# Performance work log

Measured on AMD Instinct MI355X. Metric: run time of the kernel, lower is better.

The kernel has to match this reference:

```python
import jax, jax.numpy as jnp
import numpy as np

MARGIN = 1.0
EPS = 1e-11


def setup_inputs() -> dict:
    key = jax.random.key(0)
    k1, k2, k3 = jax.random.split(key, 3)
    B, D, C = 8192, 512, 128
    features = jax.random.normal(k1, (B, D), dtype=jnp.float32)
    labels = jax.random.randint(k2, (B,), 0, C, dtype=jnp.int64)
    neg_u = jax.random.uniform(k3, (B,), dtype=jnp.float32)
    return {"features": features, "labels": labels, "neg_u": neg_u}


def reference(features, labels, neg_u):
    n = features.shape[0]
    sq = jnp.sum(features * features, axis=1)  # [n]
    d2 = sq[:, None] + sq[None, :] - 2.0 * (features @ features.T)
    dist = jnp.sqrt(jnp.clip(d2, EPS, None))  # [n, n]

    same = labels[:, None] == labels[None, :]
    eye = jnp.eye(n, dtype=bool)
    pos_mask = same & ~eye           # valid positives per anchor
    neg_mask = ~same                 # valid negatives per anchor
    n_neg = neg_mask.sum(axis=1)     # [n]

    # deterministic "random" negative: pick the floor(u * n_neg)-th negative
    # (stable argsort puts negatives first, preserving original order)
    order = jnp.argsort(jnp.where(neg_mask, 0, 1), axis=1, stable=True)  # [n, n]
    k = jnp.floor(neg_u * n_neg.astype(neg_u.dtype)).astype(jnp.int32)
    k = jnp.clip(k, 0, jnp.maximum(n_neg - 1, 0).astype(jnp.int32))
    neg_idx = jnp.take_along_axis(order, k[:, None], axis=1)[:, 0]       # [n]
    neg_dist = dist[jnp.arange(n), neg_idx]                               # [n]

    # MarginRankingLoss(y=1): max(0, margin + pos_dist - neg_dist), per (anchor, pos) pair
    valid = pos_mask & (n_neg > 0)[:, None]
    per_pair = jnp.maximum(MARGIN + dist - neg_dist[:, None], 0.0)
    counter = valid.sum()
    total = jnp.where(valid, per_pair, 0.0).sum()
    return total / counter.astype(total.dtype)
```

## Files before the change

### kernel.cpp

```cpp
#include <hip/hip_runtime.h>
#include <hip/hip_bf16.h>
#include <cstdint>

#define NN 8192
#define DD 512
#define NC 128

typedef unsigned short u16;
typedef __attribute__((ext_vector_type(8))) short short8;
typedef __attribute__((ext_vector_type(4))) float f32x4;

#define AS1 __attribute__((address_space(1)))
#define AS3 __attribute__((address_space(3)))

#define FB_OFF   ((size_t)0)
#define SQ_OFF   (FB_OFF + (size_t)NN*DD*2)
#define ND_OFF   (SQ_OFF + (size_t)NN*4)
#define ACC_OFF  (ND_OFF + (size_t)NN*4)
#define CC_OFF   (ACC_OFF + 64)
#define POS_OFF  (CC_OFF + 1024)

__global__ __launch_bounds__(256) void k_prep(const float* __restrict__ F,
    u16* __restrict__ Fb, float* __restrict__ sq, int* __restrict__ accz) {
  if (blockIdx.x == 0 && threadIdx.x < 16) accz[threadIdx.x] = 0;
  const int wid = threadIdx.x >> 6, lane = threadIdx.x & 63;
  const int row = blockIdx.x * 4 + wid;
  const float* fr = F + (size_t)row * DD + lane * 8;
  float4 v0 = *(const float4*)fr;
  float4 v1 = *(const float4*)(fr + 4);
  float s = v0.x*v0.x + v0.y*v0.y + v0.z*v0.z + v0.w*v0.w
          + v1.x*v1.x + v1.y*v1.y + v1.z*v1.z + v1.w*v1.w;
  #pragma unroll
  for (int o = 32; o; o >>= 1) s += __shfl_xor(s, o);
  float t[8] = {v0.x, v0.y, v0.z, v0.w, v1.x, v1.y, v1.z, v1.w};
  unsigned p[8];
  #pragma unroll
  for (int e = 0; e < 8; ++e) {
    unsigned b = __float_as_uint(t[e]);
    b += 0x7fffu + ((b >> 16) & 1u);
    p[e] = b >> 16;
  }
  uint4 w;
  w.x = p[0] | (p[1] << 16); w.y = p[2] | (p[3] << 16);
  w.z = p[4] | (p[5] << 16); w.w = p[6] | (p[7] << 16);
  *(uint4*)(Fb + (size_t)row * DD + lane * 8) = w;
  if (lane == 0) sq[row] = s;
}

__global__ __launch_bounds__(256) void k_classpos(const int* __restrict__ labels,
    int* __restrict__ cc, int* __restrict__ pos, int* __restrict__ cnt) {
  const int c = blockIdx.x;
  const int wid = threadIdx.x >> 6, lane = threadIdx.x & 63;
  __shared__ int wcnt[4], woff[4];
  const int base0 = wid * 2048;
  int cw = 0;
  for (int b = 0; b < 2048; b += 64)
    cw += __popcll(__ballot(labels[base0 + b + lane] == c));
  if (lane == 0) wcnt[wid] = cw;
  __syncthreads();
  if (threadIdx.x == 0) {
    int o = 0;
    #pragma unroll
    for (int w = 0; w < 4; ++w) { woff[w] = o; o += wcnt[w]; }
    cc[c] = o;
    if (o < NN) atomicAdd(cnt, o * (o - 1));
  }
  __syncthreads();
  int off = woff[wid];
  for (int b = 0; b < 2048; b += 64) {
    const int idx = base0 + b + lane;
    const int hit = (labels[idx] == c);
    const unsigned long long m = __ballot(hit);
    if (hit) pos[c * 128 + off + __popcll(m & ((1ull << lane) - 1ull))] = idx;
    off += __popcll(m);
  }
  __syncthreads();
  const int nc = cc[c];
  for (int t = nc + threadIdx.x; t < 128; t += 256) pos[c * 128 + t] = 0;
}

__global__ __launch_bounds__(256) void k_neg2(const float* __restrict__ F,
    const float* __restrict__ sq, const int* __restrict__ labels,
    const float* __restrict__ negu, const int* __restrict__ cc,
    const int* __restrict__ pos, float* __restrict__ nd) {
  const int wid = threadIdx.x >> 6, lane = threadIdx.x & 63;
  const int i = blockIdx.x * 4 + wid;
  const int c = labels[i];
  const int nc = cc[c];
  const int n_neg = NN - nc;
  if (n_neg <= 0) { if (lane == 0) nd[i] = __builtin_inff(); return; }
  int k = (int)floorf(negu[i] * (float)n_neg);
  k = k < 0 ? 0 : (k > n_neg - 1 ? n_neg - 1 : k);
  const int* pc = pos + c * 128;
  const int p0 = pc[lane], p1 = pc[64 + lane];
  const int t = __popcll(__ballot((lane < nc) && (p0 - lane <= k)))
              + __popcll(__ballot((64 + lane < nc) && (p1 - (64 + lane) <= k)));
  const int j = k + t;
  const float* fi = F + (size_t)i * DD + lane * 8;
  const float* fj = F + (size_t)j * DD + lane * 8;
  float4 a0 = *(const float4*)fi, a1 = *(const float4*)(fi + 4);
  float4 b0 = *(const float4*)fj, b1 = *(const float4*)(fj + 4);
  float d = a0.x*b0.x + a0.y*b0.y + a0.z*b0.z + a0.w*b0.w
          + a1.x*b1.x + a1.y*b1.y + a1.z*b1.z + a1.w*b1.w;
  #pragma unroll
  for (int o = 32; o; o >>= 1) d += __shfl_xor(d, o);
  if (lane == 0) nd[i] = sqrtf(fmaxf(sq[i] + sq[j] - 2.0f * d, 1e-11f));
}

__global__ __launch_bounds__(256) void k_cls(const u16* __restrict__ Fb,
    const float* __restrict__ sq, const float* __restrict__ nd,
    const int* __restrict__ cc, const int* __restrict__ pos,
    float* __restrict__ accf, float* __restrict__ out) {
  const int c = blockIdx.x;
  __shared__ __align__(16) u16 P[2][128 * 64];
  __shared__ int posc[128];
  __shared__ float red[4];
  const int tid = threadIdx.x, wid = tid >> 6, lane = tid & 63;
  const int nc = cc[c];
  if (tid < 128) posc[tid] = pos[c * 128 + tid];
  __syncthreads();
  if (nc >= 2) {
    const int wr = wid >> 1, wc = wid & 1;
    const int r16 = lane & 15, gg = lane >> 4;

    int grow[4];
    #pragma unroll
    for (int s = 0; s < 4; ++s) grow[s] = posc[wid * 32 + s * 8 + (lane >> 3)];
    const int swzg = (((lane & 7) ^ (lane >> 3)) << 4);
    const char* fb = (const char*)Fb;

    f32x4 acc[4][4];
    #pragma unroll
    for (int m = 0; m < 4; ++m)
      #pragma unroll
      for (int n = 0; n < 4; ++n)
        #pragma unroll
        for (int q = 0; q < 4; ++q) acc[m][n][q] = 0.0f;

    #define STAGE(buf, kstep) do {                                            \
      const int kb_ = (kstep) * 128;                                          \
      _Pragma("unroll")                                                       \
      for (int s_ = 0; s_ < 4; ++s_)                                          \
        __builtin_amdgcn_global_load_lds(                                     \
          (const AS1 void*)(fb + (size_t)grow[s_] * 1024 + kb_ + swzg),       \
          (AS3 void*)(&P[buf][(wid * 32 + s_ * 8) * 64]), 16, 0, 0);          \
    } while (0)

    STAGE(0, 0);
    __syncthreads();
    for (int t = 0; t < 8; ++t) {
      if (t < 7) STAGE((t + 1) & 1, t + 1);
      const u16* p = P[t & 1];
      #pragma unroll
      for (int ks = 0; ks < 2; ++ks) {
        short8 af[4], bf[4];
        #pragma unroll
        for (int m = 0; m < 4; ++m) {
          const int row = wr * 64 + m * 16 + r16;
          const int gl = (ks * 4 + gg) ^ (row & 7);
          af[m] = *(const short8*)&p[row * 64 + gl * 8];
        }
        #pragma unroll
        for (int n = 0; n < 4; ++n) {
          const int row = wc * 64 + n * 16 + r16;
          const int gl = (ks * 4 + gg) ^ (row & 7);
          bf[n] = *(const short8*)&p[row * 64 + gl * 8];
        }
        #pragma unroll
        for (int m = 0; m < 4; ++m)
          #pragma unroll
          for (int n = 0; n < 4; ++n)
            acc[m][n] = __builtin_amdgcn_mfma_f32_16x16x32_bf16(af[m], bf[n], acc[m][n], 0, 0, 0);
      }
      __syncthreads();
    }

    float lsum = 0.0f;
    int njv[4], jv[4]; float sqj[4];
    #pragma unroll
    for (int n = 0; n < 4; ++n) {
      const int nj = wc * 64 + n * 16 + r16;
      njv[n] = nj; jv[n] = posc[nj]; sqj[n] = sq[jv[n]];
    }
    #pragma unroll
    for (int m = 0; m < 4; ++m) {
      #pragma unroll
      for (int q = 0; q < 4; ++q) {
        const int mi = wr * 64 + m * 16 + gg * 4 + q;
        const int i = posc[mi];
        const float sqi = sq[i], ndi = nd[i];
        const bool vi = mi < nc;
        #pragma unroll
        for (int n = 0; n < 4; ++n) {
          const float g = acc[m][n][q];
          const float dist = sqrtf(fmaxf(sqi + sqj[n] - 2.0f * g, 1e-11f));
          if (vi & (njv[n] < nc) & (mi != njv[n]))
            lsum += fmaxf(1.0f + dist - ndi, 0.0f);
        }
      }
    }
    #pragma unroll
    for (int o = 32; o; o >>= 1) lsum += __shfl_xor(lsum, o);
    if (lane == 0) red[wid] = lsum;
    __syncthreads();
    if (tid == 0) atomicAdd(accf, red[0] + red[1] + red[2] + red[3]);
  }
  if (tid == 0) {
    __threadfence();
    int* done = (int*)accf + 2;
    if (atomicAdd(done, 1) == NC - 1) {
      const float tot = atomicAdd(accf, 0.0f);
      const int n = *(volatile int*)((int*)accf + 1);
      out[0] = tot / (float)n;
    }
  }
}

extern "C" void kernel_launch(void* const* d_in, const int* in_sizes, int n_in,
                              void* d_out, int out_size, void* d_ws, size_t ws_size,
                              hipStream_t stream) {
  const float* F = (const float*)d_in[0];
  const int* labels = (const int*)d_in[1];
  const float* negu = (const float*)d_in[2];
  char* ws = (char*)d_ws;
  u16*   Fb    = (u16*)(ws + FB_OFF);
  float* sq    = (float*)(ws + SQ_OFF);
  float* nd    = (float*)(ws + ND_OFF);
  float* accf  = (float*)(ws + ACC_OFF);
  int*   cnt   = (int*)(ws + ACC_OFF + 4);
  int*   cc    = (int*)(ws + CC_OFF);
  int*   pos   = (int*)(ws + POS_OFF);

  k_prep    <<<NN / 4, 256, 0, stream>>>(F, Fb, sq, (int*)accf);
  k_classpos<<<NC,    256, 0, stream>>>(labels, cc, pos, cnt);
  k_neg2    <<<NN / 4, 256, 0, stream>>>(F, sq, labels, negu, cc, pos, nd);
  k_cls     <<<NC,    256, 0, stream>>>(Fb, sq, nd, cc, pos, accf, (float*)d_out);
}
```

Baseline: 40.10 us.

## Merge prep and class-position kernels; load full class tile into LDS once

The bf16 conversion/row-norm kernel and the per-class position-building kernel are merged into one launch, using separate block ranges, which removes one kernel launch and its serialization gap. In the per-class Gram kernel, the double-buffered K-staged pipeline is replaced by a single bulk load of the whole 128x512 bf16 tile into 128 KB of LDS, followed by one barrier and an uninterrupted MFMA loop. This drops the per-step barriers but gives up overlap between loads and compute, and the large LDS footprint limits occupancy to one block per CU.

```diff
diff --git a/kernel.cpp b/kernel.cpp
--- a/kernel.cpp
+++ b/kernel.cpp
@@ -20,63 +20,63 @@
 #define CC_OFF   (ACC_OFF + 64)
 #define POS_OFF  (CC_OFF + 1024)
 
-__global__ __launch_bounds__(256) void k_prep(const float* __restrict__ F,
-    u16* __restrict__ Fb, float* __restrict__ sq, int* __restrict__ accz) {
-  if (blockIdx.x == 0 && threadIdx.x < 16) accz[threadIdx.x] = 0;
+__global__ __launch_bounds__(256) void k_pc(const float* __restrict__ F,
+    const int* __restrict__ labels, u16* __restrict__ Fb,
+    float* __restrict__ sq, int* __restrict__ cc, int* __restrict__ pos,
+    int* __restrict__ cnt, int* __restrict__ accz) {
   const int wid = threadIdx.x >> 6, lane = threadIdx.x & 63;
-  const int row = blockIdx.x * 4 + wid;
-  const float* fr = F + (size_t)row * DD + lane * 8;
-  float4 v0 = *(const float4*)fr;
-  float4 v1 = *(const float4*)(fr + 4);
-  float s = v0.x*v0.x + v0.y*v0.y + v0.z*v0.z + v0.w*v0.w
-          + v1.x*v1.x + v1.y*v1.y + v1.z*v1.z + v1.w*v1.w;
-  #pragma unroll
-  for (int o = 32; o; o >>= 1) s += __shfl_xor(s, o);
-  float t[8] = {v0.x, v0.y, v0.z, v0.w, v1.x, v1.y, v1.z, v1.w};
-  unsigned p[8];
-  #pragma unroll
-  for (int e = 0; e < 8; ++e) {
-    unsigned b = __float_as_uint(t[e]);
-    b += 0x7fffu + ((b >> 16) & 1u);
-    p[e] = b >> 16;
+  if (blockIdx.x < 2048) {
+    if (blockIdx.x == 0 && threadIdx.x < 16) accz[threadIdx.x] = 0;
+    const int row = blockIdx.x * 4 + wid;
+    const float* fr = F + (size_t)row * DD + lane * 8;
+    float4 v0 = *(const float4*)fr;
+    float4 v1 = *(const float4*)(fr + 4);
+    float s = v0.x*v0.x + v0.y*v0.y + v0.z*v0.z + v0.w*v0.w
+            + v1.x*v1.x + v1.y*v1.y + v1.z*v1.z + v1.w*v1.w;
+    #pragma unroll
+    for (int o = 32; o; o >>= 1) s += __shfl_xor(s, o);
+    float t[8] = {v0.x, v0.y, v0.z, v0.w, v1.x, v1.y, v1.z, v1.w};
+    unsigned p[8];
+    #pragma unroll
+    for (int e = 0; e < 8; ++e) {
+      unsigned b = __float_as_uint(t[e]);
+      b += 0x7fffu + ((b >> 16) & 1u);
+      p[e] = b >> 16;
+    }
+    uint4 w;
+    w.x = p[0] | (p[1] << 16); w.y = p[2] | (p[3] << 16);
+    w.z = p[4] | (p[5] << 16); w.w = p[6] | (p[7] << 16);
+    *(uint4*)(Fb + (size_t)row * DD + lane * 8) = w;
+    if (lane == 0) sq[row] = s;
+  } else {
+    const int c = blockIdx.x - 2048;
+    __shared__ int wcnt[4], woff[4];
+    const int base0 = wid * 2048;
+    int cw = 0;
+    for (int b = 0; b < 2048; b += 64)
+      cw += __popcll(__ballot(labels[base0 + b + lane] == c));
+    if (lane == 0) wcnt[wid] = cw;
+    __syncthreads();
+    if (threadIdx.x == 0) {
+      int o = 0;
+      #pragma unroll
+      for (int w = 0; w < 4; ++w) { woff[w] = o; o += wcnt[w]; }
+      cc[c] = o;
+      if (o < NN) atomicAdd(cnt, o * (o - 1));
+    }
+    __syncthreads();
+    int off = woff[wid];
+    for (int b = 0; b < 2048; b += 64) {
+      const int idx = base0 + b + lane;
+      const int hit = (labels[idx] == c);
+      const unsigned long long m = __ballot(hit);
+      if (hit) pos[c * 128 + off + __popcll(m & ((1ull << lane) - 1ull))] = idx;
+      off += __popcll(m);
+    }
+    __syncthreads();
+    const int nc = cc[c];
+    for (int t = nc + threadIdx.x; t < 128; t += 256) pos[c * 128 + t] = 0;
   }
-  uint4 w;
-  w.x = p[0] | (p[1] << 16); w.y = p[2] | (p[3] << 16);
-  w.z = p[4] | (p[5] << 16); w.w = p[6] | (p[7] << 16);
-  *(uint4*)(Fb + (size_t)row * DD + lane * 8) = w;
-  if (lane == 0) sq[row] = s;
-}
-
-__global__ __launch_bounds__(256) void k_classpos(const int* __restrict__ labels,
-    int* __restrict__ cc, int* __restrict__ pos, int* __restrict__ cnt) {
-  const int c = blockIdx.x;
-  const int wid = threadIdx.x >> 6, lane = threadIdx.x & 63;
-  __shared__ int wcnt[4], woff[4];
-  const int base0 = wid * 2048;
-  int cw = 0;
-  for (int b = 0; b < 2048; b += 64)
-    cw += __popcll(__ballot(labels[base0 + b + lane] == c));
-  if (lane == 0) wcnt[wid] = cw;
-  __syncthreads();
-  if (threadIdx.x == 0) {
-    int o = 0;
-    #pragma unroll
-    for (int w = 0; w < 4; ++w) { woff[w] = o; o += wcnt[w]; }
-    cc[c] = o;
-    if (o < NN) atomicAdd(cnt, o * (o - 1));
-  }
-  __syncthreads();
-  int off = woff[wid];
-  for (int b = 0; b < 2048; b += 64) {
-    const int idx = base0 + b + lane;
-    const int hit = (labels[idx] == c);
-    const unsigned long long m = __ballot(hit);
-    if (hit) pos[c * 128 + off + __popcll(m & ((1ull << lane) - 1ull))] = idx;
-    off += __popcll(m);
-  }
-  __syncthreads();
-  const int nc = cc[c];
-  for (int t = nc + threadIdx.x; t < 128; t += 256) pos[c * 128 + t] = 0;
 }
 
 __global__ __launch_bounds__(256) void k_neg2(const float* __restrict__ F,
@@ -112,7 +112,7 @@
     const int* __restrict__ cc, const int* __restrict__ pos,
     float* __restrict__ accf, float* __restrict__ out) {
   const int c = blockIdx.x;
-  __shared__ __align__(16) u16 P[2][128 * 64];
+  __shared__ __align__(16) u16 P[128 * 512];
   __shared__ int posc[128];
   __shared__ float red[4];
   const int tid = threadIdx.x, wid = tid >> 6, lane = tid & 63;
@@ -122,12 +122,16 @@
   if (nc >= 2) {
     const int wr = wid >> 1, wc = wid & 1;
     const int r16 = lane & 15, gg = lane >> 4;
-
-    int grow[4];
-    #pragma unroll
-    for (int s = 0; s < 4; ++s) grow[s] = posc[wid * 32 + s * 8 + (lane >> 3)];
-    const int swzg = (((lane & 7) ^ (lane >> 3)) << 4);
     const char* fb = (const char*)Fb;
+
+    #pragma unroll 8
+    for (int s = 0; s < 32; ++s) {
+      const int row = wid * 32 + s;
+      const int gr = posc[row];
+      __builtin_amdgcn_global_load_lds(
+          (const AS1 void*)(fb + (size_t)gr * 1024 + ((lane ^ (s & 7)) << 4)),
+          (AS3 void*)(&P[row * 512]), 16, 0, 0);
+    }
 
     f32x4 acc[4][4];
     #pragma unroll
@@ -137,42 +141,27 @@
         #pragma unroll
         for (int q = 0; q < 4; ++q) acc[m][n][q] = 0.0f;
 
-    #define STAGE(buf, kstep) do {                                            \
-      const int kb_ = (kstep) * 128;                                          \
-      _Pragma("unroll")                                                       \
-      for (int s_ = 0; s_ < 4; ++s_)                                          \
-        __builtin_amdgcn_global_load_lds(                                     \
-          (const AS1 void*)(fb + (size_t)grow[s_] * 1024 + kb_ + swzg),       \
-          (AS3 void*)(&P[buf][(wid * 32 + s_ * 8) * 64]), 16, 0, 0);          \
-    } while (0)
-
-    STAGE(0, 0);
-    __syncthreads();
-    for (int t = 0; t < 8; ++t) {
-      if (t < 7) STAGE((t + 1) & 1, t + 1);
-      const u16* p = P[t & 1];
-      #pragma unroll
-      for (int ks = 0; ks < 2; ++ks) {
-        short8 af[4], bf[4];
+    __syncthreads();
+    #pragma unroll 4
+    for (int t = 0; t < 16; ++t) {
+      short8 af[4], bf[4];
+      #pragma unroll
+      for (int m = 0; m < 4; ++m) {
+        const int row = wr * 64 + m * 16 + r16;
+        const int gl = (t * 4 + gg) ^ (row & 7);
+        af[m] = *(const short8*)&P[row * 512 + gl * 8];
+      }
+      #pragma unroll
+      for (int n = 0; n < 4; ++n) {
+        const int row = wc * 64 + n * 16 + r16;
+        const int gl = (t * 4 + gg) ^ (row & 7);
+        bf[n] = *(const short8*)&P[row * 512 + gl * 8];
+      }
+      #pragma unroll
+      for (int m = 0; m < 4; ++m)
         #pragma unroll
-        for (int m = 0; m < 4; ++m) {
-          const int row = wr * 64 + m * 16 + r16;
-          const int gl = (ks * 4 + gg) ^ (row & 7);
-          af[m] = *(const short8*)&p[row * 64 + gl * 8];
-        }
-        #pragma unroll
-        for (int n = 0; n < 4; ++n) {
-          const int row = wc * 64 + n * 16 + r16;
-          const int gl = (ks * 4 + gg) ^ (row & 7);
-          bf[n] = *(const short8*)&p[row * 64 + gl * 8];
-        }
-        #pragma unroll
-        for (int m = 0; m < 4; ++m)
-          #pragma unroll
-          for (int n = 0; n < 4; ++n)
-            acc[m][n] = __builtin_amdgcn_mfma_f32_16x16x32_bf16(af[m], bf[n], acc[m][n], 0, 0, 0);
-      }
-      __syncthreads();
+        for (int n = 0; n < 4; ++n)
+          acc[m][n] = __builtin_amdgcn_mfma_f32_16x16x32_bf16(af[m], bf[n], acc[m][n], 0, 0, 0);
     }
 
     float lsum = 0.0f;
@@ -231,8 +220,7 @@
   int*   cc    = (int*)(ws + CC_OFF);
   int*   pos   = (int*)(ws + POS_OFF);
 
-  k_prep    <<<NN / 4, 256, 0, stream>>>(F, Fb, sq, (int*)accf);
-  k_classpos<<<NC,    256, 0, stream>>>(labels, cc, pos, cnt);
-  k_neg2    <<<NN / 4, 256, 0, stream>>>(F, sq, labels, negu, cc, pos, nd);
-  k_cls     <<<NC,    256, 0, stream>>>(Fb, sq, nd, cc, pos, accf, (float*)d_out);
-}
+  k_pc  <<<2048 + NC, 256, 0, stream>>>(F, labels, Fb, sq, cc, pos, cnt, (int*)accf);
+  k_neg2<<<NN / 4,    256, 0, stream>>>(F, sq, labels, negu, cc, pos, nd);
+  k_cls <<<NC,        256, 0, stream>>>(Fb, sq, nd, cc, pos, accf, (float*)d_out);
+}
```

After: 35.55 us. 1.13x faster.
